# Kernel tuning notes

Hardware: AMD Instinct MI355X
Metric: run time of the kernel (lower is better)

The kernel has to match this reference:

```python
import jax, jax.numpy as jnp
import numpy as np

B, D, C, H, L = 32768, 64, 64, 1024, 6
EPS = 1e-5
NIN = (D - D // 2) + C  # unchanged half + cond = 96
SPLIT = D // 2          # 32


def setup_inputs() -> dict:
    key = jax.random.key(0)
    ks = jax.random.split(key, 12)
    s = 0.05
    return {
        "z": jax.random.normal(ks[0], (B, D), jnp.float32),
        "cond": jax.random.normal(ks[1], (B, C), jnp.float32),
        "W1": jax.random.normal(ks[2], (L, NIN, H), jnp.float32) * s,
        "b1": jax.random.normal(ks[3], (L, H), jnp.float32) * s,
        "W2": jax.random.normal(ks[4], (L, H, H), jnp.float32) * s,
        "b2": jax.random.normal(ks[5], (L, H), jnp.float32) * s,
        "Ws": jax.random.normal(ks[6], (L, H, SPLIT), jnp.float32) * s,
        "bs": jax.random.normal(ks[7], (L, SPLIT), jnp.float32) * s,
        "Wt": jax.random.normal(ks[8], (L, H, SPLIT), jnp.float32) * s,
        "bt": jax.random.normal(ks[9], (L, SPLIT), jnp.float32) * s,
        "bn_w": 1.0 + 0.1 * jax.random.normal(ks[10], (L, D), jnp.float32),
        "bn_b": 0.1 * jax.random.normal(ks[11], (L, D), jnp.float32),
    }


def reference(z, cond, W1, b1, W2, b2, Ws, bs, Wt, bt, bn_w, bn_b):
    x = z
    log_det = jnp.zeros((z.shape[0],), z.dtype)
    for i in range(L):
        # 'even' mask keeps even indices on even layers, odd indices otherwise
        if i % 2 == 0:
            keep, chg = np.arange(0, D, 2), np.arange(1, D, 2)
        else:
            keep, chg = np.arange(1, D, 2), np.arange(0, D, 2)
        # 2-layer MLP on [x_keep, cond]
        h = jax.nn.relu(jnp.concatenate([x[:, keep], cond], axis=1) @ W1[i] + b1[i])
        h = jax.nn.relu(h @ W2[i] + b2[i])
        log_s = jnp.tanh(h @ Ws[i] + bs[i])          # (B, SPLIT)
        t = h @ Wt[i] + bt[i]                         # (B, SPLIT)
        x2t = x[:, chg] * jnp.exp(log_s) + t
        x = jnp.zeros_like(x).at[:, keep].set(x[:, keep]).at[:, chg].set(x2t)
        log_det = log_det + log_s.sum(axis=1)
        # BatchNorm1d, training mode: batch mean / biased variance, eps=1e-5
        mean = x.mean(axis=0)
        var = x.var(axis=0)
        x = (x - mean) * jax.lax.rsqrt(var + EPS) * bn_w[i] + bn_b[i]
        log_det = log_det + jnp.log(jnp.abs(bn_w[i])).sum()
    return x, log_det
```

## Files before the change

kernel.cpp:

```cpp
#include <hip/hip_runtime.h>
#include <math.h>

#define BB 32768
#define DD 64
#define CC 64
#define HH 1024
#define LL 6
#define SPLIT 32
#define NIN 96
#define EPSV 1e-5f

typedef short short8 __attribute__((ext_vector_type(8)));
typedef float f32x4 __attribute__((ext_vector_type(4)));
typedef unsigned short u16;

__device__ __forceinline__ u16 f2bf(float f) {
    union { float f; unsigned int u; } c; c.f = f;
    unsigned int u = c.u + 0x7FFFu + ((c.u >> 16) & 1u);
    return (u16)(u >> 16);
}

__device__ __forceinline__ void gl_lds16(const u16* g, u16* l) {
    __builtin_amdgcn_global_load_lds(
        (const __attribute__((address_space(1))) unsigned int*)g,
        (__attribute__((address_space(3))) unsigned int*)l, 16, 0, 0);
}

__global__ void transpose_cvt_kernel(const float* __restrict__ src, u16* __restrict__ dst,
                                     int R, int C, int Rpad,
                                     long long sstride, long long dstride)
{
    __shared__ float tile[32][33];
    const float* s = src + (size_t)blockIdx.z * sstride;
    u16* d = dst + (size_t)blockIdx.z * dstride;
    int r0 = blockIdx.x * 32, c0 = blockIdx.y * 32;
    int tc = threadIdx.x & 31, tr = threadIdx.x >> 5;
#pragma unroll
    for (int i = 0; i < 4; ++i) {
        int r = r0 + tr + i * 8;
        tile[tr + i * 8][tc] = (r < R) ? s[(size_t)r * C + c0 + tc] : 0.f;
    }
    __syncthreads();
#pragma unroll
    for (int i = 0; i < 4; ++i) {
        int cc = tr + i * 8;
        d[(size_t)(c0 + cc) * Rpad + r0 + tc] = f2bf(tile[tc][cc]);
    }
}

__global__ __launch_bounds__(256)
void init_ain_cond_kernel(const float* __restrict__ cond, u16* __restrict__ Ain)
{
    int t = blockIdx.x * 256 + threadIdx.x;
    int c = t % 96, r = t / 96;
    Ain[(size_t)r * 128 + 32 + c] = (c < CC) ? f2bf(cond[(size_t)r * CC + c]) : (u16)0;
}

__global__ __launch_bounds__(256)
void build_keep_kernel(const float* __restrict__ x, u16* __restrict__ Ain, int keep_off)
{
    int t = blockIdx.x * 256 + threadIdx.x;
    int c = t & 31, r = t >> 5;
    Ain[(size_t)r * 128 + c] = f2bf(x[(size_t)r * DD + 2 * c + keep_off]);
}

__global__ __launch_bounds__(512, 4)
void gemm_tiled(const u16* __restrict__ A,
                const u16* __restrict__ Bt,
                const float* __restrict__ bias,
                u16* __restrict__ Cc,
                int K)
{
    __shared__ u16 sA[2][8 * 512];
    __shared__ u16 sB[2][16 * 512];

    const int t = threadIdx.x;
    const int w = t >> 6, lane = t & 63;
    const int lane16 = lane & 15, quad = lane >> 4;
    const int wm = w >> 2, wn = w & 3;

    int id = blockIdx.x;
    int nby = gridDim.x >> 2;
    int xcd = id & 7, slot = id >> 3;
    int bx = slot & 3, byq = slot >> 2;
    int by = xcd * (nby >> 3) + byq;
    const int bm = by * 128, bn = bx * 256;

    const int niter = K >> 5;

    auto stage = [&](int it, int buf) {
        int k0 = it * 32;
#pragma unroll
        for (int e3 = 0; e3 < 3; ++e3) {
            int e = w + e3 * 8;
            if (e < 8) {
                const u16* g = A + (size_t)(bm + e * 16 + lane16) * K + k0 + quad * 8;
                gl_lds16(g, &sA[buf][e * 512]);
            } else {
                int j = e - 8;
                const u16* g = Bt + (size_t)(bn + j * 16 + lane16) * K + k0 + quad * 8;
                gl_lds16(g, &sB[buf][j * 512]);
            }
        }
    };

    f32x4 acc[4][4];
#pragma unroll
    for (int a = 0; a < 4; ++a)
#pragma unroll
        for (int b = 0; b < 4; ++b) acc[a][b] = (f32x4){0.f, 0.f, 0.f, 0.f};

    stage(0, 0);
    for (int it = 0; it < niter; ++it) {
        const int buf = it & 1;
        __syncthreads();
        if (it + 1 < niter) stage(it + 1, buf ^ 1);
        short8 af[4], bf[4];
#pragma unroll
        for (int a = 0; a < 4; ++a)
            af[a] = *(const short8*)(&sA[buf][(wm * 4 + a) * 512 + lane * 8]);
#pragma unroll
        for (int b = 0; b < 4; ++b)
            bf[b] = *(const short8*)(&sB[buf][(wn * 4 + b) * 512 + lane * 8]);
#pragma unroll
        for (int a = 0; a < 4; ++a)
#pragma unroll
            for (int b = 0; b < 4; ++b)
                acc[a][b] = __builtin_amdgcn_mfma_f32_16x16x32_bf16(af[a], bf[b], acc[a][b], 0, 0, 0);
    }
    __syncthreads();

    constexpr int ES = 72;
    float bv[4];
#pragma unroll
    for (int b = 0; b < 4; ++b) bv[b] = bias[bn + wn * 64 + b * 16 + lane16];
    u16* scr = ((u16*)sB) + w * (16 * ES);
#pragma unroll
    for (int a = 0; a < 4; ++a) {
#pragma unroll
        for (int b = 0; b < 4; ++b)
#pragma unroll
            for (int r = 0; r < 4; ++r) {
                float v = fmaxf(acc[a][b][r] + bv[b], 0.f);
                scr[(quad * 4 + r) * ES + b * 16 + lane16] = f2bf(v);
            }
#pragma unroll
        for (int ch = 0; ch < 2; ++ch) {
            int row = ch * 8 + (lane >> 3), colc = (lane & 7) * 8;
            short8 v = *(const short8*)(scr + row * ES + colc);
            *(short8*)(Cc + (size_t)(bm + wm * 64 + a * 16 + row) * 1024 + bn + wn * 64 + colc) = v;
        }
    }
}

__global__ __launch_bounds__(256)
void gemm3_coupling(const u16* __restrict__ A,
                    const u16* __restrict__ Bt,
                    const float* __restrict__ bs, const float* __restrict__ bt,
                    float* __restrict__ x, float* __restrict__ log_det,
                    float* __restrict__ stat_sum, float* __restrict__ stat_sumsq,
                    int keep_off, int row0)
{
    constexpr int K = HH;
    constexpr int ST_STRIDE = 66;
    __shared__ float sst[64 * ST_STRIDE];
    __shared__ float ssum[4][64], ssum2[4][64];
    u16* lds = (u16*)sst;

    const int t = threadIdx.x;
    const int w = t >> 6, lane = t & 63;
    const int lane16 = lane & 15, quad = lane >> 4;
    const int wm = w >> 1, wn = w & 1;
    const int bm = blockIdx.x * 64;

    u16* ldsA = lds;
    u16* ldsB = lds + 8 * 512;

    f32x4 acc[2][2];
#pragma unroll
    for (int a = 0; a < 2; ++a)
#pragma unroll
        for (int b = 0; b < 2; ++b) acc[a][b] = (f32x4){0.f, 0.f, 0.f, 0.f};

    for (int k0 = 0; k0 < K; k0 += 64) {
        for (int e = w; e < 8; e += 4) {
            int s = e >> 2, i = e & 3;
            const u16* g = A + (size_t)(bm + i * 16 + lane16) * K + (k0 + s * 32 + quad * 8);
            gl_lds16(g, ldsA + e * 512);
        }
        for (int e = w; e < 8; e += 4) {
            int s = e >> 2, j = e & 3;
            const u16* g = Bt + (size_t)(j * 16 + lane16) * K + (k0 + s * 32 + quad * 8);
            gl_lds16(g, ldsB + e * 512);
        }
        __syncthreads();
#pragma unroll
        for (int s = 0; s < 2; ++s) {
            short8 af[2], bfr[2];
#pragma unroll
            for (int a = 0; a < 2; ++a)
                af[a] = *(const short8*)(ldsA + ((s * 4 + wm * 2 + a) * 64 + lane) * 8);
#pragma unroll
            for (int b = 0; b < 2; ++b)
                bfr[b] = *(const short8*)(ldsB + ((s * 4 + wn * 2 + b) * 64 + lane) * 8);
#pragma unroll
            for (int a = 0; a < 2; ++a)
#pragma unroll
                for (int b = 0; b < 2; ++b)
                    acc[a][b] = __builtin_amdgcn_mfma_f32_16x16x32_bf16(af[a], bfr[b], acc[a][b], 0, 0, 0);
        }
        __syncthreads();
    }

#pragma unroll
    for (int a = 0; a < 2; ++a)
#pragma unroll
        for (int b = 0; b < 2; ++b)
#pragma unroll
            for (int r = 0; r < 4; ++r) {
                int row = wm * 32 + a * 16 + quad * 4 + r;
                int col = wn * 32 + b * 16 + lane16;
                sst[row * ST_STRIDE + col] = acc[a][b][r];
            }
    __syncthreads();

    const int f = lane;
    const bool is_chg = ((f & 1) != keep_off);
    const int j = f >> 1;
    float bsj = 0.f, btj = 0.f;
    if (is_chg) { bsj = bs[j]; btj = bt[j]; }

    float lsum = 0.f, lsum2 = 0.f;
    for (int i = 0; i < 16; ++i) {
        int crow = w * 16 + i;
        int grow = row0 + bm + crow;
        float xv = x[(size_t)grow * DD + f];
        float ld = 0.f;
        if (is_chg) {
            float s_raw = sst[crow * ST_STRIDE + j];
            float t_raw = sst[crow * ST_STRIDE + SPLIT + j];
            float ls = tanhf(s_raw + bsj);
            float tv = t_raw + btj;
            xv = xv * expf(ls) + tv;
            x[(size_t)grow * DD + f] = xv;
            ld = ls;
        }
        for (int off = 32; off > 0; off >>= 1) ld += __shfl_down(ld, off, 64);
        if (f == 0) log_det[grow] += ld;
        lsum  += xv;
        lsum2 += xv * xv;
    }

    ssum[w][f]  = lsum;
    ssum2[w][f] = lsum2;
    __syncthreads();
    if (t < 64) {
        float a = ssum[0][t] + ssum[1][t] + ssum[2][t] + ssum[3][t];
        float b = ssum2[0][t] + ssum2[1][t] + ssum2[2][t] + ssum2[3][t];
        atomicAdd(stat_sum + t, a);
        atomicAdd(stat_sumsq + t, b);
    }
}

__global__ void finalize_kernel(const float* __restrict__ stat_sum, const float* __restrict__ stat_sumsq,
                                const float* __restrict__ bn_w, const float* __restrict__ bn_b,
                                float* __restrict__ scale, float* __restrict__ shift,
                                float* __restrict__ cbuf)
{
    int f = threadIdx.x;
    const float invB = 1.f / (float)BB;
    float mean = stat_sum[f] * invB;
    float var  = stat_sumsq[f] * invB - mean * mean;
    float inv  = rsqrtf(var + EPSV);
    float w    = bn_w[f];
    float sc   = inv * w;
    scale[f] = sc;
    shift[f] = bn_b[f] - mean * sc;
    float lg = logf(fabsf(w));
    for (int off = 32; off > 0; off >>= 1) lg += __shfl_down(lg, off, 64);
    if (f == 0) cbuf[0] = lg;
}

__global__ __launch_bounds__(256)
void normalize_kernel(const float* __restrict__ xin, float* __restrict__ xout,
                      const float* __restrict__ scale, const float* __restrict__ shift,
                      const float* __restrict__ cbuf, float* __restrict__ log_det,
                      u16* __restrict__ Ain, int off_next)
{
    int idx = blockIdx.x * blockDim.x + threadIdx.x;
    int f0 = (idx & 15) * 4;
    int row = idx >> 4;
    float4 v = ((const float4*)xin)[idx];
    v.x = v.x * scale[f0 + 0] + shift[f0 + 0];
    v.y = v.y * scale[f0 + 1] + shift[f0 + 1];
    v.z = v.z * scale[f0 + 2] + shift[f0 + 2];
    v.w = v.w * scale[f0 + 3] + shift[f0 + 3];
    ((float4*)xout)[idx] = v;
    if ((idx & 15) == 0) log_det[row] += cbuf[0];
    if (Ain) {
        float a0 = off_next ? v.y : v.x;
        float a1 = off_next ? v.w : v.z;
        ushort2 u; u.x = f2bf(a0); u.y = f2bf(a1);
        *(ushort2*)(Ain + (size_t)row * 128 + (f0 >> 1)) = u;
    }
}

extern "C" void kernel_launch(void* const* d_in, const int* in_sizes, int n_in,
                              void* d_out, int out_size, void* d_ws, size_t ws_size,
                              hipStream_t stream)
{
    const float* z    = (const float*)d_in[0];
    const float* cond = (const float*)d_in[1];
    const float* W1   = (const float*)d_in[2];
    const float* b1   = (const float*)d_in[3];
    const float* W2   = (const float*)d_in[4];
    const float* b2   = (const float*)d_in[5];
    const float* Ws   = (const float*)d_in[6];
    const float* bs   = (const float*)d_in[7];
    const float* Wt   = (const float*)d_in[8];
    const float* bt   = (const float*)d_in[9];
    const float* bn_w = (const float*)d_in[10];
    const float* bn_b = (const float*)d_in[11];

    float* out_x  = (float*)d_out;
    float* out_ld = out_x + (size_t)BB * DD;

    char* p = (char*)d_ws;
    size_t used = 0;
    auto alloc = [&](size_t bytes) { void* q = p + used; used += (bytes + 255) & ~(size_t)255; return q; };

    float* xbuf = (float*)alloc((size_t)BB * DD * 4);
    u16*   w1t  = (u16*)alloc((size_t)LL * HH * 128 * 2);
    u16*   w2t  = (u16*)alloc((size_t)LL * HH * HH * 2);
    u16*   wstt = (u16*)alloc((size_t)LL * 64 * HH * 2);
    u16*   Ain  = (u16*)alloc((size_t)BB * 128 * 2);
    float* stat_sum   = (float*)alloc(64 * 4);
    float* stat_sumsq = (float*)alloc(64 * 4);
    float* scalev     = (float*)alloc(64 * 4);
    float* shiftv     = (float*)alloc(64 * 4);
    float* cbuf       = (float*)alloc(64 * 4);

    int CH = BB;
    while (CH > 8192 && used + (size_t)CH * 4096 + 4096 > ws_size) CH >>= 1;
    u16* h1 = (u16*)alloc((size_t)CH * HH * 2);
    u16* h2 = (u16*)alloc((size_t)CH * HH * 2);

    hipMemcpyAsync(xbuf, z, (size_t)BB * DD * sizeof(float), hipMemcpyDeviceToDevice, stream);
    hipMemsetAsync(out_ld, 0, (size_t)BB * sizeof(float), stream);

    transpose_cvt_kernel<<<dim3(128/32, HH/32, LL), 256, 0, stream>>>(
        W1, w1t, NIN, HH, 128, (long long)NIN * HH, (long long)HH * 128);
    transpose_cvt_kernel<<<dim3(HH/32, HH/32, LL), 256, 0, stream>>>(
        W2, w2t, HH, HH, HH, (long long)HH * HH, (long long)HH * HH);
    transpose_cvt_kernel<<<dim3(HH/32, SPLIT/32, LL), 256, 0, stream>>>(
        Ws, wstt, HH, SPLIT, HH, (long long)HH * SPLIT, (long long)64 * HH);
    transpose_cvt_kernel<<<dim3(HH/32, SPLIT/32, LL), 256, 0, stream>>>(
        Wt, wstt + (size_t)SPLIT * HH, HH, SPLIT, HH, (long long)HH * SPLIT, (long long)64 * HH);

    init_ain_cond_kernel<<<BB * 96 / 256, 256, 0, stream>>>(cond, Ain);
    build_keep_kernel<<<BB * 32 / 256, 256, 0, stream>>>(xbuf, Ain, 0);

    for (int l = 0; l < LL; ++l) {
        const int off = l & 1;
        hipMemsetAsync(stat_sum, 0, 2 * 64 * sizeof(float), stream);

        for (int c = 0; c < BB / CH; ++c) {
            const int row0 = c * CH;

            gemm_tiled<<<(CH / 128) * 4, 512, 0, stream>>>(
                Ain + (size_t)row0 * 128, w1t + (size_t)l * HH * 128,
                b1 + (size_t)l * HH, h1, 128);

            gemm_tiled<<<(CH / 128) * 4, 512, 0, stream>>>(
                h1, w2t + (size_t)l * HH * HH,
                b2 + (size_t)l * HH, h2, HH);

            gemm3_coupling<<<CH / 64, 256, 0, stream>>>(
                h2, wstt + (size_t)l * 64 * HH,
                bs + (size_t)l * SPLIT, bt + (size_t)l * SPLIT,
                xbuf, out_ld, stat_sum, stat_sumsq, off, row0);
        }

        finalize_kernel<<<1, 64, 0, stream>>>(
            stat_sum, stat_sumsq, bn_w + (size_t)l * DD, bn_b + (size_t)l * DD,
            scalev, shiftv, cbuf);

        float* xout = (l == LL - 1) ? out_x : xbuf;
        u16* ain_next = (l < LL - 1) ? Ain : nullptr;
        normalize_kernel<<<(BB * DD / 4) / 256, 256, 0, stream>>>(
            xbuf, xout, scalev, shiftv, cbuf, out_ld, ain_next, (l + 1) & 1);
    }
}
```

Before: 1.128 ms.

## Shrink main GEMM tile to 128x128, enlarge coupling tile, fuse BN finalize

The main bf16 GEMM moves from 512-thread blocks with 128x256 tiles to 256-thread blocks with 128x128 tiles, doubling the block count and halving LDS per block. This may improve occupancy and load balance, at the cost of more redundant A-tile loads. The coupling GEMM now handles 128 rows per 512-thread block, so each block loads the small weight matrix half as often overall and issues fewer atomics. The one-thread-block finalize kernel is folded into the normalize kernel, which recomputes scale and shift per block and saves a launch.

```diff
diff --git a/kernel.cpp b/kernel.cpp
--- a/kernel.cpp
+++ b/kernel.cpp
@@ -64,7 +64,7 @@
     Ain[(size_t)r * 128 + c] = f2bf(x[(size_t)r * DD + 2 * c + keep_off]);
 }
 
-__global__ __launch_bounds__(512, 4)
+__global__ __launch_bounds__(256, 4)
 void gemm_tiled(const u16* __restrict__ A,
                 const u16* __restrict__ Bt,
                 const float* __restrict__ bias,
@@ -72,27 +72,27 @@
                 int K)
 {
     __shared__ u16 sA[2][8 * 512];
-    __shared__ u16 sB[2][16 * 512];
+    __shared__ u16 sB[2][8 * 512];
 
     const int t = threadIdx.x;
     const int w = t >> 6, lane = t & 63;
     const int lane16 = lane & 15, quad = lane >> 4;
-    const int wm = w >> 2, wn = w & 3;
+    const int wm = w >> 1, wn = w & 1;
 
     int id = blockIdx.x;
-    int nby = gridDim.x >> 2;
+    int nby = gridDim.x >> 3;
     int xcd = id & 7, slot = id >> 3;
-    int bx = slot & 3, byq = slot >> 2;
+    int bx = slot & 7, byq = slot >> 3;
     int by = xcd * (nby >> 3) + byq;
-    const int bm = by * 128, bn = bx * 256;
+    const int bm = by * 128, bn = bx * 128;
 
     const int niter = K >> 5;
 
     auto stage = [&](int it, int buf) {
         int k0 = it * 32;
 #pragma unroll
-        for (int e3 = 0; e3 < 3; ++e3) {
-            int e = w + e3 * 8;
+        for (int i = 0; i < 4; ++i) {
+            int e = w + i * 4;
             if (e < 8) {
                 const u16* g = A + (size_t)(bm + e * 16 + lane16) * K + k0 + quad * 8;
                 gl_lds16(g, &sA[buf][e * 512]);
@@ -134,7 +134,7 @@
     float bv[4];
 #pragma unroll
     for (int b = 0; b < 4; ++b) bv[b] = bias[bn + wn * 64 + b * 16 + lane16];
-    u16* scr = ((u16*)sB) + w * (16 * ES);
+    u16* scr = ((u16*)sA) + w * (16 * ES);
 #pragma unroll
     for (int a = 0; a < 4; ++a) {
 #pragma unroll
@@ -153,7 +153,7 @@
     }
 }
 
-__global__ __launch_bounds__(256)
+__global__ __launch_bounds__(512)
 void gemm3_coupling(const u16* __restrict__ A,
                     const u16* __restrict__ Bt,
                     const float* __restrict__ bs, const float* __restrict__ bt,
@@ -163,18 +163,18 @@
 {
     constexpr int K = HH;
     constexpr int ST_STRIDE = 66;
-    __shared__ float sst[64 * ST_STRIDE];
-    __shared__ float ssum[4][64], ssum2[4][64];
+    __shared__ float sst[128 * ST_STRIDE];
+    __shared__ float ssum[8][64], ssum2[8][64];
     u16* lds = (u16*)sst;
 
     const int t = threadIdx.x;
     const int w = t >> 6, lane = t & 63;
     const int lane16 = lane & 15, quad = lane >> 4;
     const int wm = w >> 1, wn = w & 1;
-    const int bm = blockIdx.x * 64;
+    const int bm = blockIdx.x * 128;
 
     u16* ldsA = lds;
-    u16* ldsB = lds + 8 * 512;
+    u16* ldsB = lds + 16 * 512;
 
     f32x4 acc[2][2];
 #pragma unroll
@@ -183,15 +183,15 @@
         for (int b = 0; b < 2; ++b) acc[a][b] = (f32x4){0.f, 0.f, 0.f, 0.f};
 
     for (int k0 = 0; k0 < K; k0 += 64) {
-        for (int e = w; e < 8; e += 4) {
-            int s = e >> 2, i = e & 3;
+        for (int e = w; e < 16; e += 8) {
+            int s = e >> 3, i = e & 7;
             const u16* g = A + (size_t)(bm + i * 16 + lane16) * K + (k0 + s * 32 + quad * 8);
             gl_lds16(g, ldsA + e * 512);
         }
-        for (int e = w; e < 8; e += 4) {
-            int s = e >> 2, j = e & 3;
+        {
+            int s = w >> 2, j = w & 3;
             const u16* g = Bt + (size_t)(j * 16 + lane16) * K + (k0 + s * 32 + quad * 8);
-            gl_lds16(g, ldsB + e * 512);
+            gl_lds16(g, ldsB + w * 512);
         }
         __syncthreads();
 #pragma unroll
@@ -199,10 +199,10 @@
             short8 af[2], bfr[2];
 #pragma unroll
             for (int a = 0; a < 2; ++a)
-                af[a] = *(const short8*)(ldsA + ((s * 4 + wm * 2 + a) * 64 + lane) * 8);
+                af[a] = *(const short8*)(ldsA + ((s * 8 + wm * 2 + a) * 512) + lane * 8);
 #pragma unroll
             for (int b = 0; b < 2; ++b)
-                bfr[b] = *(const short8*)(ldsB + ((s * 4 + wn * 2 + b) * 64 + lane) * 8);
+                bfr[b] = *(const short8*)(ldsB + ((s * 4 + wn * 2 + b) * 512) + lane * 8);
 #pragma unroll
             for (int a = 0; a < 2; ++a)
 #pragma unroll
@@ -255,48 +255,48 @@
     ssum2[w][f] = lsum2;
     __syncthreads();
     if (t < 64) {
-        float a = ssum[0][t] + ssum[1][t] + ssum[2][t] + ssum[3][t];
-        float b = ssum2[0][t] + ssum2[1][t] + ssum2[2][t] + ssum2[3][t];
+        float a = 0.f, b = 0.f;
+#pragma unroll
+        for (int g = 0; g < 8; ++g) { a += ssum[g][t]; b += ssum2[g][t]; }
         atomicAdd(stat_sum + t, a);
         atomicAdd(stat_sumsq + t, b);
     }
 }
 
-__global__ void finalize_kernel(const float* __restrict__ stat_sum, const float* __restrict__ stat_sumsq,
-                                const float* __restrict__ bn_w, const float* __restrict__ bn_b,
-                                float* __restrict__ scale, float* __restrict__ shift,
-                                float* __restrict__ cbuf)
-{
-    int f = threadIdx.x;
-    const float invB = 1.f / (float)BB;
-    float mean = stat_sum[f] * invB;
-    float var  = stat_sumsq[f] * invB - mean * mean;
-    float inv  = rsqrtf(var + EPSV);
-    float w    = bn_w[f];
-    float sc   = inv * w;
-    scale[f] = sc;
-    shift[f] = bn_b[f] - mean * sc;
-    float lg = logf(fabsf(w));
-    for (int off = 32; off > 0; off >>= 1) lg += __shfl_down(lg, off, 64);
-    if (f == 0) cbuf[0] = lg;
-}
-
 __global__ __launch_bounds__(256)
 void normalize_kernel(const float* __restrict__ xin, float* __restrict__ xout,
-                      const float* __restrict__ scale, const float* __restrict__ shift,
-                      const float* __restrict__ cbuf, float* __restrict__ log_det,
+                      const float* __restrict__ stat_sum, const float* __restrict__ stat_sumsq,
+                      const float* __restrict__ bn_w, const float* __restrict__ bn_b,
+                      float* __restrict__ log_det,
                       u16* __restrict__ Ain, int off_next)
 {
-    int idx = blockIdx.x * blockDim.x + threadIdx.x;
+    __shared__ float sscale[64], sshift[64], scsum;
+    int t = threadIdx.x;
+    if (t < 64) {
+        const float invB = 1.f / (float)BB;
+        float mean = stat_sum[t] * invB;
+        float var  = stat_sumsq[t] * invB - mean * mean;
+        float inv  = rsqrtf(var + EPSV);
+        float wv   = bn_w[t];
+        float sc   = inv * wv;
+        sscale[t] = sc;
+        sshift[t] = bn_b[t] - mean * sc;
+        float lg = logf(fabsf(wv));
+        for (int off = 32; off > 0; off >>= 1) lg += __shfl_down(lg, off, 64);
+        if (t == 0) scsum = lg;
+    }
+    __syncthreads();
+
+    int idx = blockIdx.x * blockDim.x + t;
     int f0 = (idx & 15) * 4;
     int row = idx >> 4;
     float4 v = ((const float4*)xin)[idx];
-    v.x = v.x * scale[f0 + 0] + shift[f0 + 0];
-    v.y = v.y * scale[f0 + 1] + shift[f0 + 1];
-    v.z = v.z * scale[f0 + 2] + shift[f0 + 2];
-    v.w = v.w * scale[f0 + 3] + shift[f0 + 3];
+    v.x = v.x * sscale[f0 + 0] + sshift[f0 + 0];
+    v.y = v.y * sscale[f0 + 1] + sshift[f0 + 1];
+    v.z = v.z * sscale[f0 + 2] + sshift[f0 + 2];
+    v.w = v.w * sscale[f0 + 3] + sshift[f0 + 3];
     ((float4*)xout)[idx] = v;
-    if ((idx & 15) == 0) log_det[row] += cbuf[0];
+    if ((idx & 15) == 0) log_det[row] += scsum;
     if (Ain) {
         float a0 = off_next ? v.y : v.x;
         float a1 = off_next ? v.w : v.z;
@@ -336,9 +336,6 @@
     u16*   Ain  = (u16*)alloc((size_t)BB * 128 * 2);
     float* stat_sum   = (float*)alloc(64 * 4);
     float* stat_sumsq = (float*)alloc(64 * 4);
-    float* scalev     = (float*)alloc(64 * 4);
-    float* shiftv     = (float*)alloc(64 * 4);
-    float* cbuf       = (float*)alloc(64 * 4);
 
     int CH = BB;
     while (CH > 8192 && used + (size_t)CH * 4096 + 4096 > ws_size) CH >>= 1;
@@ -367,27 +364,25 @@
         for (int c = 0; c < BB / CH; ++c) {
             const int row0 = c * CH;
 
-            gemm_tiled<<<(CH / 128) * 4, 512, 0, stream>>>(
+            gemm_tiled<<<(CH / 128) * 8, 256, 0, stream>>>(
                 Ain + (size_t)row0 * 128, w1t + (size_t)l * HH * 128,
                 b1 + (size_t)l * HH, h1, 128);
 
-            gemm_tiled<<<(CH / 128) * 4, 512, 0, stream>>>(
+            gemm_tiled<<<(CH / 128) * 8, 256, 0, stream>>>(
                 h1, w2t + (size_t)l * HH * HH,
                 b2 + (size_t)l * HH, h2, HH);
 
-            gemm3_coupling<<<CH / 64, 256, 0, stream>>>(
+            gemm3_coupling<<<CH / 128, 512, 0, stream>>>(
                 h2, wstt + (size_t)l * 64 * HH,
                 bs + (size_t)l * SPLIT, bt + (size_t)l * SPLIT,
                 xbuf, out_ld, stat_sum, stat_sumsq, off, row0);
         }
 
-        finalize_kernel<<<1, 64, 0, stream>>>(
-            stat_sum, stat_sumsq, bn_w + (size_t)l * DD, bn_b + (size_t)l * DD,
-            scalev, shiftv, cbuf);
-
         float* xout = (l == LL - 1) ? out_x : xbuf;
         u16* ain_next = (l < LL - 1) ? Ain : nullptr;
         normalize_kernel<<<(BB * DD / 4) / 256, 256, 0, stream>>>(
-            xbuf, xout, scalev, shiftv, cbuf, out_ld, ain_next, (l + 1) & 1);
-    }
-}
+            xbuf, xout, stat_sum, stat_sumsq,
+            bn_w + (size_t)l * DD, bn_b + (size_t)l * DD,
+            out_ld, ain_next, (l + 1) & 1);
+    }
+}
```

Measured after the change: 1.286 ms. +14.0%, slower.
